# Optimization experiments

Hardware: AMD Instinct MI355X
Metric: run time of the kernel (lower is better)

## Reference

```python
import jax, jax.numpy as jnp
import numpy as np

EMBED_DIM = 384


def setup_inputs() -> dict:
    key = jax.random.key(0)
    k1, k2, k3 = jax.random.split(key, 3)
    B, P, N, C = 32, 4, 1024, EMBED_DIM
    x = jax.random.normal(k1, (B, P, N, C), dtype=jnp.float32)
    # 1x1 Conv2D on channel-last == linear on last dim; kernel [Cin, Cout]
    w_qkv = jax.random.normal(k2, (C, 1 + 2 * C), dtype=jnp.float32) * (1.0 / np.sqrt(C))
    b_qkv = jnp.zeros((1 + 2 * C,), dtype=jnp.float32)
    w_proj = jax.random.normal(k3, (C, C), dtype=jnp.float32) * (1.0 / np.sqrt(C))
    b_proj = jnp.zeros((C,), dtype=jnp.float32)
    return {"x": x, "w_qkv": w_qkv, "b_qkv": b_qkv, "w_proj": w_proj, "b_proj": b_proj}


def reference(x, w_qkv, b_qkv, w_proj, b_proj):
    C = EMBED_DIM
    # qkv pointwise conv: [B,P,N,C] @ [C, 1+2C]
    qkv = jnp.einsum('bpnc,cd->bpnd', x, w_qkv) + b_qkv
    query = qkv[..., :1]                 # [B,P,N,1]
    key_t = qkv[..., 1:1 + C]            # [B,P,N,C]
    value = qkv[..., 1 + C:]             # [B,P,N,C]
    # NOTE: softmax over the trailing axis of size 1 (faithful to source) -> all ones
    context_scores = jax.nn.softmax(query, axis=-1)
    # key * scores, reduce-sum over patch-index axis (axis=2), keepdims
    context_vector = jnp.sum(key_t * context_scores, axis=2, keepdims=True)  # [B,P,1,C]
    gated = jax.nn.relu(value) * context_vector                              # [B,P,N,C]
    out = jnp.einsum('bpnc,cd->bpnd', gated, w_proj) + b_proj
    return out
```

## Files before the change

### kernel.cpp

```cpp
#include <hip/hip_runtime.h>
#include <hip/hip_bf16.h>
#include <type_traits>
#include <utility>

#define C_     384
#define N_     1024
#define G_     128
#define QKVD   769
#define TILE_B 24576

typedef float  f32x4 __attribute__((ext_vector_type(4)));
typedef short  s16x8 __attribute__((ext_vector_type(8)));
typedef __bf16 b16x8 __attribute__((ext_vector_type(8)));

template <typename V, typename = void>
struct mfma_takes : std::false_type {};
template <typename V>
struct mfma_takes<V, std::void_t<decltype(__builtin_amdgcn_mfma_f32_16x16x32_bf16(
    std::declval<V>(), std::declval<V>(), std::declval<f32x4>(), 0, 0, 0))>>
    : std::true_type {};

using frag_t = std::conditional_t<mfma_takes<s16x8>::value, s16x8, b16x8>;

template <typename V>
__device__ __forceinline__ f32x4 mfma_bf16(V a, V b, f32x4 c) {
  return __builtin_amdgcn_mfma_f32_16x16x32_bf16(a, b, c, 0, 0, 0);
}

__device__ __forceinline__ unsigned short f2bf(float f) {
  union { float f; unsigned u; } v; v.f = f;
  unsigned r = v.u + 0x7fffu + ((v.u >> 16) & 1u);
  return (unsigned short)(r >> 16);
}
__device__ __forceinline__ unsigned pack2(float lo, float hi) {
  return (unsigned)f2bf(lo) | ((unsigned)f2bf(hi) << 16);
}

__device__ __forceinline__ void stage16(const char* g, char* lbase, int lane) {
#if __has_builtin(__builtin_amdgcn_global_load_lds)
  __builtin_amdgcn_global_load_lds(
      (const __attribute__((address_space(1))) void*)g,
      (__attribute__((address_space(3))) void*)lbase, 16, 0, 0);
#else
  *(uint4*)(lbase + lane * 16) = *(const uint4*)g;
#endif
}

__global__ __launch_bounds__(512) void k_prep(
    const float* __restrict__ x, const float* __restrict__ w_qkv,
    const float* __restrict__ w_proj, char* __restrict__ xbb,
    float* __restrict__ xsum, unsigned short* __restrict__ pWv,
    unsigned short* __restrict__ pWp) {
  const int b   = blockIdx.x;
  const int tid = threadIdx.x;

  if (b < 512) {
    __shared__ float csum[C_];
    const int g = b >> 2;
    for (int c = tid; c < C_; c += 512) csum[c] = 0.f;
    __syncthreads();

    if (tid < 384) {
      const int col8 = (tid % 48) * 8;
      const int rg   = tid / 48;
      const float* xg = x + (size_t)b * 256 * C_ + col8;
      char* img = xbb + (size_t)b * 8 * TILE_B;
      float s0=0,s1=0,s2=0,s3=0,s4=0,s5=0,s6=0,s7=0;
#pragma unroll 1
      for (int im = 0; im < 8; ++im) {
#pragma unroll
        for (int j = 0; j < 4; ++j) {
          int row = rg * 4 + j;
          const float* src = xg + ((size_t)im * 32 + row) * C_;
          float4 a = *(const float4*)(src);
          float4 c = *(const float4*)(src + 4);
          uint4 w;
          w.x = pack2(a.x, a.y); w.y = pack2(a.z, a.w);
          w.z = pack2(c.x, c.y); w.w = pack2(c.z, c.w);
          *(uint4*)(img + im * TILE_B +
                    ((row * 768 + col8 * 2) ^ ((row & 7) << 4))) = w;
          s0 += a.x; s1 += a.y; s2 += a.z; s3 += a.w;
          s4 += c.x; s5 += c.y; s6 += c.z; s7 += c.w;
        }
      }
      atomicAdd(&csum[col8 + 0], s0); atomicAdd(&csum[col8 + 1], s1);
      atomicAdd(&csum[col8 + 2], s2); atomicAdd(&csum[col8 + 3], s3);
      atomicAdd(&csum[col8 + 4], s4); atomicAdd(&csum[col8 + 5], s5);
      atomicAdd(&csum[col8 + 6], s6); atomicAdd(&csum[col8 + 7], s7);
    }
    __syncthreads();
    if (tid < 384) atomicAdd(&xsum[g * C_ + tid], csum[tid]);
  } else {
    int pb   = (b - 512) * 8 + (tid >> 6);
    int mat  = pb / 288;
    int r    = pb % 288;
    int kk   = r / 24, nf = r % 24;
    int lane = tid & 63;
    int kbase = kk * 32 + (lane >> 4) * 8;
    int n     = nf * 16 + (lane & 15);
    unsigned v[4];
#pragma unroll
    for (int jj = 0; jj < 4; ++jj) {
      int k0 = kbase + jj * 2;
      float f0 = mat ? w_proj[(size_t)k0 * C_ + n]       : w_qkv[(size_t)k0 * QKVD + 385 + n];
      float f1 = mat ? w_proj[(size_t)(k0 + 1) * C_ + n] : w_qkv[(size_t)(k0 + 1) * QKVD + 385 + n];
      v[jj] = (unsigned)f2bf(f0) | ((unsigned)f2bf(f1) << 16);
    }
    unsigned short* dst = (mat ? pWp : pWv) + ((size_t)r * 64 + lane) * 8;
    uint4 w; w.x = v[0]; w.y = v[1]; w.z = v[2]; w.w = v[3];
    *(uint4*)dst = w;
  }
}

__global__ __launch_bounds__(384) void k_xsum(const float* __restrict__ x,
                                              float* __restrict__ xsum) {
  __shared__ float sh[4][C_];
  const int tid = threadIdx.x;
  const int c4  = (tid % 96) * 4;
  const int rg  = tid / 96;
  const int b   = blockIdx.x;
  const int g   = b >> 3;
  const float* p = x + ((size_t)b * 128 + (size_t)rg * 32) * C_ + c4;
  f32x4 s = {0.f, 0.f, 0.f, 0.f};
#pragma unroll 8
  for (int r = 0; r < 32; ++r) {
    float4 v = *(const float4*)(p + (size_t)r * C_);
    s.x += v.x; s.y += v.y; s.z += v.z; s.w += v.w;
  }
  *(f32x4*)&sh[rg][c4] = s;
  __syncthreads();
  if (rg == 0) {
#pragma unroll
    for (int j = 0; j < 4; ++j) {
      float v = sh[0][c4 + j] + sh[1][c4 + j] + sh[2][c4 + j] + sh[3][c4 + j];
      atomicAdd(&xsum[g * C_ + c4 + j], v);
    }
  }
}

__global__ void k_pack(const float* __restrict__ w_qkv, const float* __restrict__ w_proj,
                       unsigned short* __restrict__ pWv, unsigned short* __restrict__ pWp) {
  int bid = blockIdx.x;
  int mat = bid / 288;
  int r   = bid % 288;
  int kk = r / 24, nf = r % 24;
  int lane = threadIdx.x;
  int kbase = kk * 32 + (lane >> 4) * 8;
  int n = nf * 16 + (lane & 15);
  unsigned v[4];
#pragma unroll
  for (int jj = 0; jj < 4; ++jj) {
    int k0 = kbase + jj * 2;
    float f0 = mat ? w_proj[(size_t)k0 * C_ + n]       : w_qkv[(size_t)k0 * QKVD + 385 + n];
    float f1 = mat ? w_proj[(size_t)(k0 + 1) * C_ + n] : w_qkv[(size_t)(k0 + 1) * QKVD + 385 + n];
    v[jj] = (unsigned)f2bf(f0) | ((unsigned)f2bf(f1) << 16);
  }
  unsigned short* dst = (mat ? pWp : pWv) + ((size_t)r * 64 + lane) * 8;
  uint4 w; w.x = v[0]; w.y = v[1]; w.z = v[2]; w.w = v[3];
  *(uint4*)dst = w;
}

__global__ void k_cv(const float* __restrict__ xsum, const float* __restrict__ w_qkv,
                     const float* __restrict__ b_qkv, float* __restrict__ cv) {
  __shared__ float xs[C_];
  int g = blockIdx.x, c = threadIdx.x;
  xs[c] = xsum[g * C_ + c];
  __syncthreads();
  float acc = 0.f;
#pragma unroll 4
  for (int k = 0; k < C_; ++k) acc += xs[k] * w_qkv[k * QKVD + 1 + c];
  cv[g * C_ + c] = acc + (float)N_ * b_qkv[1 + c];
}

template <bool PRE>
__global__ __launch_bounds__(512) void k_fused(
    const float* __restrict__ x, const char* __restrict__ xbb,
    const unsigned short* __restrict__ pWv, const unsigned short* __restrict__ pWp,
    const float* __restrict__ cv, const float* __restrict__ b_qkv,
    const float* __restrict__ b_proj, float* __restrict__ out) {
  __shared__ __align__(16) char tile[32 * 768];
  __shared__ float cv_l[C_], bv_l[C_], bp_l[C_];

  const int tid  = threadIdx.x;
  const int lane = tid & 63;
  const int wv   = tid >> 6;
  const int R0   = blockIdx.x * 32;
  const int g    = R0 >> 10;

  if (tid < C_) {
    cv_l[tid] = cv[g * C_ + tid];
    bv_l[tid] = b_qkv[1 + C_ + tid];
    bp_l[tid] = b_proj[tid];
  }

  if constexpr (PRE) {
    const char* img = xbb + (size_t)blockIdx.x * TILE_B;
#pragma unroll
    for (int j = 0; j < 3; ++j) {
      int cb = (wv * 3 + j) * 1024;
      stage16(img + cb + lane * 16, tile + cb, lane);
    }
  } else {
    const float* xg = x + (size_t)R0 * C_;
#pragma unroll
    for (int j = 0; j < 3; ++j) {
      int ch  = tid + j * 512;
      int row = ch / 48;
      int c8  = (ch % 48) * 8;
      const float4* s0 = (const float4*)(xg + (size_t)row * C_ + c8);
      float4 a = s0[0], b = s0[1];
      uint4 w;
      w.x = pack2(a.x, a.y); w.y = pack2(a.z, a.w);
      w.z = pack2(b.x, b.y); w.w = pack2(b.z, b.w);
      int byte = (row * 768 + c8 * 2) ^ ((row & 7) << 4);
      *(uint4*)(tile + byte) = w;
    }
  }
  __syncthreads();

  const f32x4 zero = {0.f, 0.f, 0.f, 0.f};
  f32x4 acc[2][3];
#pragma unroll
  for (int m = 0; m < 2; ++m)
#pragma unroll
    for (int n = 0; n < 3; ++n) acc[m][n] = zero;

  for (int kk = 0; kk < 12; ++kk) {
    frag_t A[2], Bv[3];
    int kb2 = (kk * 32 + (lane >> 4) * 8) * 2;
#pragma unroll
    for (int m = 0; m < 2; ++m) {
      int row = m * 16 + (lane & 15);
      A[m] = *(const frag_t*)(tile + ((row * 768 + kb2) ^ ((row & 7) << 4)));
    }
    const unsigned short* bp_ = pWv + ((size_t)(kk * 24 + wv * 3) * 64 + lane) * 8;
#pragma unroll
    for (int n = 0; n < 3; ++n) Bv[n] = *(const frag_t*)(bp_ + (size_t)n * 64 * 8);
#pragma unroll
    for (int m = 0; m < 2; ++m)
#pragma unroll
      for (int n = 0; n < 3; ++n) acc[m][n] = mfma_bf16(A[m], Bv[n], acc[m][n]);
  }
  __syncthreads();

#pragma unroll
  for (int m = 0; m < 2; ++m) {
#pragma unroll
    for (int n = 0; n < 3; ++n) {
      int col = wv * 48 + n * 16 + (lane & 15);
      float cvv = cv_l[col], bvv = bv_l[col];
#pragma unroll
      for (int r = 0; r < 4; ++r) {
        int row = m * 16 + (lane >> 4) * 4 + r;
        float val = fmaxf(acc[m][n][r] + bvv, 0.f) * cvv;
        *(unsigned short*)(tile + ((row * 768 + col * 2) ^ ((row & 7) << 4))) = f2bf(val);
      }
    }
  }
  __syncthreads();

#pragma unroll
  for (int m = 0; m < 2; ++m)
#pragma unroll
    for (int n = 0; n < 3; ++n) acc[m][n] = zero;

  for (int kk = 0; kk < 12; ++kk) {
    frag_t A[2], Bv[3];
    int kb2 = (kk * 32 + (lane >> 4) * 8) * 2;
#pragma unroll
    for (int m = 0; m < 2; ++m) {
      int row = m * 16 + (lane & 15);
      A[m] = *(const frag_t*)(tile + ((row * 768 + kb2) ^ ((row & 7) << 4)));
    }
    const unsigned short* bp_ = pWp + ((size_t)(kk * 24 + wv * 3) * 64 + lane) * 8;
#pragma unroll
    for (int n = 0; n < 3; ++n) Bv[n] = *(const frag_t*)(bp_ + (size_t)n * 64 * 8);
#pragma unroll
    for (int m = 0; m < 2; ++m)
#pragma unroll
      for (int n = 0; n < 3; ++n) acc[m][n] = mfma_bf16(A[m], Bv[n], acc[m][n]);
  }

#pragma unroll
  for (int m = 0; m < 2; ++m) {
#pragma unroll
    for (int n = 0; n < 3; ++n) {
      int col = wv * 48 + n * 16 + (lane & 15);
      float bpv = bp_l[col];
#pragma unroll
      for (int r = 0; r < 4; ++r) {
        int row = m * 16 + (lane >> 4) * 4 + r;
        out[(size_t)(R0 + row) * C_ + col] = acc[m][n][r] + bpv;
      }
    }
  }
}

extern "C" void kernel_launch(void* const* d_in, const int* in_sizes, int n_in,
                              void* d_out, int out_size, void* d_ws, size_t ws_size,
                              hipStream_t stream) {
  const float* x      = (const float*)d_in[0];
  const float* w_qkv  = (const float*)d_in[1];
  const float* b_qkv  = (const float*)d_in[2];
  const float* w_proj = (const float*)d_in[3];
  const float* b_proj = (const float*)d_in[4];
  float* out = (float*)d_out;

  float* xsum = (float*)d_ws;
  float* cvp  = xsum + G_ * C_;
  unsigned short* pWv = (unsigned short*)(cvp + G_ * C_);
  unsigned short* pWp = pWv + C_ * C_;
  char* xbb = (char*)(pWp + C_ * C_);

  const size_t need = 983040 + (size_t)4096 * TILE_B;

  hipMemsetAsync(xsum, 0, G_ * C_ * sizeof(float), stream);

  if (ws_size >= need) {
    k_prep<<<584, 512, 0, stream>>>(x, w_qkv, w_proj, xbb, xsum, pWv, pWp);
    k_cv<<<G_, C_, 0, stream>>>(xsum, w_qkv, b_qkv, cvp);
    k_fused<true><<<4096, 512, 0, stream>>>(x, xbb, pWv, pWp, cvp, b_qkv, b_proj, out);
  } else {
    k_pack<<<576, 64, 0, stream>>>(w_qkv, w_proj, pWv, pWp);
    k_xsum<<<1024, 384, 0, stream>>>(x, xsum);
    k_cv<<<G_, C_, 0, stream>>>(xsum, w_qkv, b_qkv, cvp);
    k_fused<false><<<4096, 512, 0, stream>>>(x, xbb, pWv, pWp, cvp, b_qkv, b_proj, out);
  }
}
```

Measured before the change: 239.8 us.

## Process four tiles per block with double-buffered LDS staging and drop atomics

The fused kernel now handles four 32-row tiles per block over 1024 blocks. The next bf16 tile is prefetched into a second LDS buffer while the current one runs through both GEMMs, and biases and the context vector are held in registers. The prep kernel writes per-block partial column sums instead of global atomics, and a new cv kernel reduces the four partials, which removes the memset. This trades fewer blocks (less parallelism) and more LDS per block for hiding load latency and cutting launch and setup overhead.

```diff
diff --git a/kernel.cpp b/kernel.cpp
--- a/kernel.cpp
+++ b/kernel.cpp
@@ -49,14 +49,13 @@
 __global__ __launch_bounds__(512) void k_prep(
     const float* __restrict__ x, const float* __restrict__ w_qkv,
     const float* __restrict__ w_proj, char* __restrict__ xbb,
-    float* __restrict__ xsum, unsigned short* __restrict__ pWv,
+    float* __restrict__ xsumP, unsigned short* __restrict__ pWv,
     unsigned short* __restrict__ pWp) {
   const int b   = blockIdx.x;
   const int tid = threadIdx.x;
 
   if (b < 512) {
     __shared__ float csum[C_];
-    const int g = b >> 2;
     for (int c = tid; c < C_; c += 512) csum[c] = 0.f;
     __syncthreads();
 
@@ -89,7 +88,7 @@
       atomicAdd(&csum[col8 + 6], s6); atomicAdd(&csum[col8 + 7], s7);
     }
     __syncthreads();
-    if (tid < 384) atomicAdd(&xsum[g * C_ + tid], csum[tid]);
+    if (tid < 384) xsumP[(size_t)b * C_ + tid] = csum[tid];
   } else {
     int pb   = (b - 512) * 8 + (tid >> 6);
     int mat  = pb / 288;
@@ -110,6 +109,19 @@
     uint4 w; w.x = v[0]; w.y = v[1]; w.z = v[2]; w.w = v[3];
     *(uint4*)dst = w;
   }
+}
+
+__global__ void k_cv4(const float* __restrict__ xsumP, const float* __restrict__ w_qkv,
+                      const float* __restrict__ b_qkv, float* __restrict__ cv) {
+  __shared__ float xs[C_];
+  int g = blockIdx.x, c = threadIdx.x;
+  xs[c] = xsumP[(size_t)(g * 4 + 0) * C_ + c] + xsumP[(size_t)(g * 4 + 1) * C_ + c] +
+          xsumP[(size_t)(g * 4 + 2) * C_ + c] + xsumP[(size_t)(g * 4 + 3) * C_ + c];
+  __syncthreads();
+  float acc = 0.f;
+#pragma unroll 4
+  for (int k = 0; k < C_; ++k) acc += xs[k] * w_qkv[k * QKVD + 1 + c];
+  cv[g * C_ + c] = acc + (float)N_ * b_qkv[1 + c];
 }
 
 __global__ __launch_bounds__(384) void k_xsum(const float* __restrict__ x,
@@ -172,12 +184,132 @@
   cv[g * C_ + c] = acc + (float)N_ * b_qkv[1 + c];
 }
 
-template <bool PRE>
-__global__ __launch_bounds__(512) void k_fused(
-    const float* __restrict__ x, const char* __restrict__ xbb,
-    const unsigned short* __restrict__ pWv, const unsigned short* __restrict__ pWp,
-    const float* __restrict__ cv, const float* __restrict__ b_qkv,
-    const float* __restrict__ b_proj, float* __restrict__ out) {
+__global__ __launch_bounds__(512) void k_fused_multi(
+    const char* __restrict__ xbb, const unsigned short* __restrict__ pWv,
+    const unsigned short* __restrict__ pWp, const float* __restrict__ cv,
+    const float* __restrict__ b_qkv, const float* __restrict__ b_proj,
+    float* __restrict__ out) {
+  __shared__ __align__(16) char buf[2][TILE_B];
+  const int tid  = threadIdx.x;
+  const int lane = tid & 63;
+  const int wv   = tid >> 6;
+  const int b    = blockIdx.x;
+  const int g    = b >> 3;
+
+  float cvr[3], bvr[3], bpr[3];
+#pragma unroll
+  for (int n = 0; n < 3; ++n) {
+    int col = wv * 48 + n * 16 + (lane & 15);
+    cvr[n] = cv[g * C_ + col];
+    bvr[n] = b_qkv[1 + C_ + col];
+    bpr[n] = b_proj[col];
+  }
+
+  const char* img0 = xbb + (size_t)b * 4 * TILE_B;
+  const f32x4 zero = {0.f, 0.f, 0.f, 0.f};
+
+#pragma unroll
+  for (int j = 0; j < 3; ++j) {
+    int cb = (wv * 3 + j) * 1024;
+    stage16(img0 + cb + lane * 16, buf[0] + cb, lane);
+  }
+  __syncthreads();
+
+#pragma unroll 1
+  for (int t = 0; t < 4; ++t) {
+    const int p = t & 1;
+
+    if (t < 3) {
+      const char* src = img0 + (size_t)(t + 1) * TILE_B;
+#pragma unroll
+      for (int j = 0; j < 3; ++j) {
+        int cb = (wv * 3 + j) * 1024;
+        stage16(src + cb + lane * 16, buf[p ^ 1] + cb, lane);
+      }
+    }
+
+    f32x4 acc[2][3];
+#pragma unroll
+    for (int m = 0; m < 2; ++m)
+#pragma unroll
+      for (int n = 0; n < 3; ++n) acc[m][n] = zero;
+
+    for (int kk = 0; kk < 12; ++kk) {
+      frag_t A[2], Bv[3];
+      int kb2 = (kk * 32 + (lane >> 4) * 8) * 2;
+#pragma unroll
+      for (int m = 0; m < 2; ++m) {
+        int row = m * 16 + (lane & 15);
+        A[m] = *(const frag_t*)(buf[p] + ((row * 768 + kb2) ^ ((row & 7) << 4)));
+      }
+      const unsigned short* bp_ = pWv + ((size_t)(kk * 24 + wv * 3) * 64 + lane) * 8;
+#pragma unroll
+      for (int n = 0; n < 3; ++n) Bv[n] = *(const frag_t*)(bp_ + (size_t)n * 64 * 8);
+#pragma unroll
+      for (int m = 0; m < 2; ++m)
+#pragma unroll
+        for (int n = 0; n < 3; ++n) acc[m][n] = mfma_bf16(A[m], Bv[n], acc[m][n]);
+    }
+    __syncthreads();
+
+#pragma unroll
+    for (int m = 0; m < 2; ++m) {
+#pragma unroll
+      for (int n = 0; n < 3; ++n) {
+        int col = wv * 48 + n * 16 + (lane & 15);
+#pragma unroll
+        for (int r = 0; r < 4; ++r) {
+          int row = m * 16 + (lane >> 4) * 4 + r;
+          float val = fmaxf(acc[m][n][r] + bvr[n], 0.f) * cvr[n];
+          *(unsigned short*)(buf[p] + ((row * 768 + col * 2) ^ ((row & 7) << 4))) = f2bf(val);
+        }
+      }
+    }
+    __syncthreads();
+
+#pragma unroll
+    for (int m = 0; m < 2; ++m)
+#pragma unroll
+      for (int n = 0; n < 3; ++n) acc[m][n] = zero;
+
+    for (int kk = 0; kk < 12; ++kk) {
+      frag_t A[2], Bv[3];
+      int kb2 = (kk * 32 + (lane >> 4) * 8) * 2;
+#pragma unroll
+      for (int m = 0; m < 2; ++m) {
+        int row = m * 16 + (lane & 15);
+        A[m] = *(const frag_t*)(buf[p] + ((row * 768 + kb2) ^ ((row & 7) << 4)));
+      }
+      const unsigned short* bp_ = pWp + ((size_t)(kk * 24 + wv * 3) * 64 + lane) * 8;
+#pragma unroll
+      for (int n = 0; n < 3; ++n) Bv[n] = *(const frag_t*)(bp_ + (size_t)n * 64 * 8);
+#pragma unroll
+      for (int m = 0; m < 2; ++m)
+#pragma unroll
+        for (int n = 0; n < 3; ++n) acc[m][n] = mfma_bf16(A[m], Bv[n], acc[m][n]);
+    }
+
+#pragma unroll
+    for (int m = 0; m < 2; ++m) {
+#pragma unroll
+      for (int n = 0; n < 3; ++n) {
+        int col = wv * 48 + n * 16 + (lane & 15);
+#pragma unroll
+        for (int r = 0; r < 4; ++r) {
+          int row = m * 16 + (lane >> 4) * 4 + r;
+          out[((size_t)b * 128 + (size_t)t * 32 + row) * C_ + col] = acc[m][n][r] + bpr[n];
+        }
+      }
+    }
+    __syncthreads();
+  }
+}
+
+__global__ __launch_bounds__(512) void k_fused_fb(
+    const float* __restrict__ x, const unsigned short* __restrict__ pWv,
+    const unsigned short* __restrict__ pWp, const float* __restrict__ cv,
+    const float* __restrict__ b_qkv, const float* __restrict__ b_proj,
+    float* __restrict__ out) {
   __shared__ __align__(16) char tile[32 * 768];
   __shared__ float cv_l[C_], bv_l[C_], bp_l[C_];
 
@@ -192,15 +324,7 @@
     bv_l[tid] = b_qkv[1 + C_ + tid];
     bp_l[tid] = b_proj[tid];
   }
-
-  if constexpr (PRE) {
-    const char* img = xbb + (size_t)blockIdx.x * TILE_B;
-#pragma unroll
-    for (int j = 0; j < 3; ++j) {
-      int cb = (wv * 3 + j) * 1024;
-      stage16(img + cb + lane * 16, tile + cb, lane);
-    }
-  } else {
+  {
     const float* xg = x + (size_t)R0 * C_;
 #pragma unroll
     for (int j = 0; j < 3; ++j) {
@@ -306,24 +430,24 @@
   const float* b_proj = (const float*)d_in[4];
   float* out = (float*)d_out;
 
-  float* xsum = (float*)d_ws;
-  float* cvp  = xsum + G_ * C_;
+  float* xsumP = (float*)d_ws;
+  float* cvp   = xsumP + 512 * C_;
   unsigned short* pWv = (unsigned short*)(cvp + G_ * C_);
   unsigned short* pWp = pWv + C_ * C_;
   char* xbb = (char*)(pWp + C_ * C_);
 
-  const size_t need = 983040 + (size_t)4096 * TILE_B;
-
-  hipMemsetAsync(xsum, 0, G_ * C_ * sizeof(float), stream);
+  const size_t need = (size_t)(512 + G_) * C_ * 4 + (size_t)C_ * C_ * 2 * 2 +
+                      (size_t)4096 * TILE_B;
 
   if (ws_size >= need) {
-    k_prep<<<584, 512, 0, stream>>>(x, w_qkv, w_proj, xbb, xsum, pWv, pWp);
-    k_cv<<<G_, C_, 0, stream>>>(xsum, w_qkv, b_qkv, cvp);
-    k_fused<true><<<4096, 512, 0, stream>>>(x, xbb, pWv, pWp, cvp, b_qkv, b_proj, out);
+    k_prep<<<584, 512, 0, stream>>>(x, w_qkv, w_proj, xbb, xsumP, pWv, pWp);
+    k_cv4<<<G_, C_, 0, stream>>>(xsumP, w_qkv, b_qkv, cvp);
+    k_fused_multi<<<1024, 512, 0, stream>>>(xbb, pWv, pWp, cvp, b_qkv, b_proj, out);
   } else {
+    hipMemsetAsync(xsumP, 0, G_ * C_ * sizeof(float), stream);
     k_pack<<<576, 64, 0, stream>>>(w_qkv, w_proj, pWv, pWp);
-    k_xsum<<<1024, 384, 0, stream>>>(x, xsum);
-    k_cv<<<G_, C_, 0, stream>>>(xsum, w_qkv, b_qkv, cvp);
-    k_fused<false><<<4096, 512, 0, stream>>>(x, xbb, pWv, pWp, cvp, b_qkv, b_proj, out);
-  }
-}
+    k_xsum<<<1024, 384, 0, stream>>>(x, xsumP);
+    k_cv<<<G_, C_, 0, stream>>>(xsumP, w_qkv, b_qkv, cvp);
+    k_fused_fb<<<4096, 512, 0, stream>>>(x, pWv, pWp, cvp, b_qkv, b_proj, out);
+  }
+}
```

After: 524.5 us. 2.19x slower.
